# Kernel optimization log

Hardware: AMD Instinct MI355X
Metric: run time of the kernel (lower is better)

Reference implementation:

```python
import jax, jax.numpy as jnp
import numpy as np

DIM = 1024
NUM_HEADS = 16
HEAD_DIM = DIM // NUM_HEADS
SCALE = HEAD_DIM ** -0.5
B, LQ, LK = 2, 2048, 2048


def setup_inputs() -> dict:
    key = jax.random.key(0)
    ks = jax.random.split(key, 12)
    init = 1.0 / np.sqrt(DIM)  # ~ torch Linear default scale
    inp = {
        "q": jax.random.normal(ks[0], (B, LQ, DIM), jnp.float32),
        "k": jax.random.normal(ks[1], (B, LK, DIM), jnp.float32),
        "v": jax.random.normal(ks[2], (B, LK, DIM), jnp.float32),
        "kv_mask": jnp.ones((B, LK), jnp.int32),
        "Wq": jax.random.uniform(ks[3], (DIM, DIM), jnp.float32, -init, init),
        "bq": jax.random.uniform(ks[4], (DIM,), jnp.float32, -init, init),
        "Wk": jax.random.uniform(ks[5], (DIM, DIM), jnp.float32, -init, init),
        "bk": jax.random.uniform(ks[6], (DIM,), jnp.float32, -init, init),
        "Wv": jax.random.uniform(ks[7], (DIM, DIM), jnp.float32, -init, init),
        "bv": jax.random.uniform(ks[8], (DIM,), jnp.float32, -init, init),
        "Wo": jax.random.uniform(ks[9], (DIM, DIM), jnp.float32, -init, init),
        "bo": jax.random.uniform(ks[10], (DIM,), jnp.float32, -init, init),
    }
    return inp


def reference(q, k, v, kv_mask, Wq, bq, Wk, bk, Wv, bv, Wo, bo):
    Bq, Lq, D = q.shape
    Lk = k.shape[1]
    H, Hd = NUM_HEADS, HEAD_DIM
    # projections (torch Linear: x @ W.T + b); split heads -> [B, H, L, Hd]
    qh = (q @ Wq.T + bq).reshape(Bq, Lq, H, Hd).transpose(0, 2, 1, 3)
    kh = (k @ Wk.T + bk).reshape(Bq, Lk, H, Hd).transpose(0, 2, 1, 3)
    vh = (v @ Wv.T + bv).reshape(Bq, Lk, H, Hd).transpose(0, 2, 1, 3)
    # scores [B, H, Lq, Lk]
    attn = jnp.einsum("bhqd,bhkd->bhqk", qh, kh) * SCALE
    mask = (kv_mask != 0)[:, None, None, :]
    attn = jnp.where(mask, attn, -jnp.inf)
    attn = jax.nn.softmax(attn, axis=-1)
    # dropout is identity at inference (p applied only in train mode)
    out = jnp.einsum("bhqk,bhkd->bhqd", attn, vh)
    out = out.transpose(0, 2, 1, 3).reshape(Bq, Lq, D)
    return out @ Wo.T + bo
```

## Files before the change

kernel.cpp:

```cpp
#include <hip/hip_runtime.h>
#include <stdint.h>

typedef unsigned short u16;
typedef __attribute__((ext_vector_type(8))) __bf16 bf16x8;
typedef __attribute__((ext_vector_type(4))) float f32x4;

#define DIM 1024
#define NH 16
#define HD 64
#define BSZ 2
#define LQ 2048
#define LK 2048
#define SCALE_LOG2E 0.18033688011112043f
#define MNEG -3.0e38f


static __device__ __forceinline__ float b2f(u16 u) {
  union { uint32_t i; float f; } v; v.i = ((uint32_t)u) << 16; return v.f;
}
static __device__ __forceinline__ u16 f2b(float f) {
  uint32_t x = __float_as_uint(f);
  return (u16)((x + 0x7fffu + ((x >> 16) & 1u)) >> 16);
}
static __device__ __forceinline__ uint32_t pk2r(float lo, float hi) {
  uint32_t a = __float_as_uint(lo) + 0x8000u;
  uint32_t b = __float_as_uint(hi) + 0x8000u;
  return __builtin_amdgcn_perm(b, a, 0x07060302u);
}
static __device__ __forceinline__ f32x4 zero4() {
  f32x4 z; z[0] = 0.f; z[1] = 0.f; z[2] = 0.f; z[3] = 0.f; return z;
}
static __device__ __forceinline__ float exp2c(float s) {
  return exp2f(fminf(s, 30.0f));
}
static __device__ __forceinline__ void gload_lds16(const u16* g, u16* l) {
  __builtin_amdgcn_global_load_lds(
      (const __attribute__((address_space(1))) void*)g,
      (__attribute__((address_space(3))) void*)l, 16, 0, 0);
}

__global__ void mask_allvalid(const int* __restrict__ kvmask, int* allv) {
  int b = blockIdx.x;
  int base = b * LK + threadIdx.x * 8;
  int ok = 1;
#pragma unroll
  for (int j = 0; j < 8; ++j) ok &= (kvmask[base + j] != 0);
  unsigned long long m = __ballot(ok != 0);
  if ((threadIdx.x & 63) == 0 && m != ~0ULL) atomicAnd(&allv[b], 0);
}

struct ConvArgs {
  const float* src[11];
  long long cum[12];
  u16* dst;
};

__global__ void convert_inputs(ConvArgs ca) {
  long long c = (long long)blockIdx.x * blockDim.x + threadIdx.x;
  long long e0 = c * 8;
  if (e0 >= ca.cum[11]) return;
  int s = 0;
  while (e0 >= ca.cum[s + 1]) ++s;
  const float* sp = ca.src[s] + (e0 - ca.cum[s]);
  union { uint4 v; uint32_t w[4]; } t;
#pragma unroll
  for (int j = 0; j < 4; ++j) t.w[j] = pk2r(sp[2 * j], sp[2 * j + 1]);
  *(uint4*)(ca.dst + e0) = t.v;
}

struct GemmArgs {
  const u16* X[3];
  const u16* W[3];
  const u16* Bias[3];
  void* Y[3];
  float osc[3];
  int f32out;
  int vtz;
};

__global__ __launch_bounds__(256, 2) void gemm_bt_bias(GemmArgs ga) {
  const int K = DIM, N = DIM;
  __shared__ u16 smem[17408];
  u16* const Al = smem;
  u16* const Bl = smem + 8192;
  const int tid = threadIdx.x;
  const int wave = tid >> 6, lane = tid & 63;
  const int wm = wave >> 1, wn = wave & 1;
  const int lrow = lane & 15, quad = lane >> 4;
  const int z = blockIdx.z;
  const u16* X = ga.X[z];
  const u16* W = ga.W[z];
  const u16* Bias = ga.Bias[z];
  const float osc = ga.osc[z];
  const int m0 = blockIdx.x * 128;
  const int n0 = blockIdx.y * 128;

  f32x4 acc[4][4];
#pragma unroll
  for (int i = 0; i < 4; ++i)
#pragma unroll
    for (int j = 0; j < 4; ++j) acc[i][j] = zero4();

  const int cbase = wave * 256;
  for (int k0 = 0; k0 < K; k0 += 64) {
    __syncthreads();
#pragma unroll
    for (int i = 0; i < 4; ++i) {
      int c = cbase + i * 64 + lane;
      int row = c >> 3, colb = c & 7;
      gload_lds16(X + (size_t)(m0 + row) * K + k0 + colb * 8,
                  &Al[(cbase + i * 64) * 8]);
      gload_lds16(W + (size_t)(n0 + row) * K + k0 + colb * 8,
                  &Bl[(cbase + i * 64) * 8]);
    }
    __syncthreads();
#pragma unroll
    for (int ks = 0; ks < 2; ++ks) {
      bf16x8 af[4], bfr[4];
#pragma unroll
      for (int t = 0; t < 4; ++t)
        af[t] = *(const bf16x8*)&Al[(wm * 64 + t * 16 + lrow) * 64 + ks * 32 + quad * 8];
#pragma unroll
      for (int t = 0; t < 4; ++t)
        bfr[t] = *(const bf16x8*)&Bl[(wn * 64 + t * 16 + lrow) * 64 + ks * 32 + quad * 8];
#pragma unroll
      for (int mt = 0; mt < 4; ++mt)
#pragma unroll
        for (int nt = 0; nt < 4; ++nt)
          acc[mt][nt] = __builtin_amdgcn_mfma_f32_16x16x32_bf16(af[mt], bfr[nt], acc[mt][nt], 0, 0, 0);
    }
  }

  if (z == ga.vtz) {
    u16* Yv = (u16*)ga.Y[z];
    u16* const VT = smem;
    __syncthreads();
#pragma unroll
    for (int nt = 0; nt < 4; ++nt) {
      int colL = wn * 64 + nt * 16 + lrow;
      float bv = b2f(Bias[n0 + colL]);
#pragma unroll
      for (int mt = 0; mt < 4; ++mt) {
        int keyL = wm * 64 + mt * 16 + quad * 4;
        uint2 w;
        w.x = pk2r((acc[mt][nt][0] + bv) * osc, (acc[mt][nt][1] + bv) * osc);
        w.y = pk2r((acc[mt][nt][2] + bv) * osc, (acc[mt][nt][3] + bv) * osc);
        *(uint2*)&VT[colL * 136 + keyL] = w;
      }
    }
    __syncthreads();
    const int bb = m0 >> 11, key0 = m0 & 2047;
#pragma unroll
    for (int i = 0; i < 8; ++i) {
      int c = i * 256 + tid;
      int colL = c >> 4, k8 = c & 15;
      int hh = (n0 + colL) >> 6, dd = (n0 + colL) & 63;
      *(uint4*)(Yv + ((size_t)(bb * NH + hh) * HD + dd) * LK + key0 + k8 * 8) =
          *(const uint4*)&VT[colL * 136 + k8 * 8];
    }
  } else if (ga.f32out) {
    float* Yf = (float*)ga.Y[z];
#pragma unroll
    for (int nt = 0; nt < 4; ++nt) {
      int col = n0 + wn * 64 + nt * 16 + lrow;
      float bv = b2f(Bias[col]);
#pragma unroll
      for (int mt = 0; mt < 4; ++mt) {
        int rowb = m0 + wm * 64 + mt * 16 + quad * 4;
#pragma unroll
        for (int r = 0; r < 4; ++r)
          Yf[(size_t)(rowb + r) * N + col] = (acc[mt][nt][r] + bv) * osc;
      }
    }
  } else {
    u16* Yv = (u16*)ga.Y[z];
#pragma unroll
    for (int nt = 0; nt < 4; ++nt) {
      int col = n0 + wn * 64 + nt * 16 + lrow;
      float bv = b2f(Bias[col]);
#pragma unroll
      for (int mt = 0; mt < 4; ++mt) {
        int rowb = m0 + wm * 64 + mt * 16 + quad * 4;
#pragma unroll
        for (int r = 0; r < 4; ++r)
          Yv[(size_t)(rowb + r) * N + col] = f2b((acc[mt][nt][r] + bv) * osc);
      }
    }
  }
}

__global__ __launch_bounds__(256, 2) void attn_fused(
    const u16* __restrict__ qp, const u16* __restrict__ kp,
    const u16* __restrict__ vpt, const int* __restrict__ kvmask,
    const int* __restrict__ allv, u16* __restrict__ op) {
  __shared__ u16 Kl[128 * 72];
  __shared__ u16 Vt[64 * 136];
  __shared__ u16 Pp[4][32 * 40];
  __shared__ float Ml[128];
  const int tid = threadIdx.x;
  const int wave = tid >> 6, lane = tid & 63;
  const int lrow = lane & 15, quad = lane >> 4;
  const int bh = blockIdx.y;
  const int b = bh >> 4, h = bh & 15;
  const int q0 = blockIdx.x * 128;
  const bool av = (allv[b] != 0);

  const u16* qbase = qp + (size_t)b * LQ * DIM + h * HD;
  const u16* kbase = kp + (size_t)b * LK * DIM + h * HD;
  const u16* vtb = vpt + (size_t)(b * NH + h) * HD * LK;
  const int* mbase = kvmask + b * LK;
  const int wq0 = q0 + wave * 32;

  bf16x8 qf[2][2];
#pragma unroll
  for (int mt = 0; mt < 2; ++mt)
#pragma unroll
    for (int ks = 0; ks < 2; ++ks)
      qf[mt][ks] = *(const bf16x8*)(qbase + (size_t)(wq0 + mt * 16 + lrow) * DIM + ks * 32 + quad * 8);

  f32x4 acco[2][4];
  float lsum[2];
#pragma unroll
  for (int mt = 0; mt < 2; ++mt) {
#pragma unroll
    for (int dt = 0; dt < 4; ++dt) acco[mt][dt] = zero4();
    lsum[mt] = 0.0f;
  }

  const int kr_row = tid >> 3, kr_cb = (tid & 7) * 8;
  const int vr_d = tid >> 4, vr_k8 = (tid & 15) * 8;
  const u16* kptr = kbase + (size_t)kr_row * DIM + kr_cb;
  const u16* vptr = vtb + (size_t)vr_d * LK + vr_k8;
  u16* klds = &Kl[kr_row * 72 + kr_cb];
  u16* vlds = &Vt[vr_d * 136 + vr_k8];

  uint4 kr0, kr1, kr2, kr3, vr0, vr1, vr2, vr3;

  kr0 = *(const uint4*)(kptr);
  kr1 = *(const uint4*)(kptr + (size_t)32 * DIM);
  kr2 = *(const uint4*)(kptr + (size_t)64 * DIM);
  kr3 = *(const uint4*)(kptr + (size_t)96 * DIM);
  vr0 = *(const uint4*)(vptr);
  vr1 = *(const uint4*)(vptr + (size_t)16 * LK);
  vr2 = *(const uint4*)(vptr + (size_t)32 * LK);
  vr3 = *(const uint4*)(vptr + (size_t)48 * LK);
  *(uint4*)(klds) = kr0;
  *(uint4*)(klds + 32 * 72) = kr1;
  *(uint4*)(klds + 64 * 72) = kr2;
  *(uint4*)(klds + 96 * 72) = kr3;
  *(uint4*)(vlds) = vr0;
  *(uint4*)(vlds + 16 * 136) = vr1;
  *(uint4*)(vlds + 32 * 136) = vr2;
  *(uint4*)(vlds + 48 * 136) = vr3;
  if (!av && tid < 128) Ml[tid] = mbase[tid] ? 0.0f : MNEG;

  for (int kc = 0; kc < LK; kc += 128) {
    __syncthreads();
    const bool more = (kc + 128) < LK;

    if (more) {
      const u16* kp2 = kptr + (size_t)(kc + 128) * DIM;
      const u16* vp2 = vptr + (kc + 128);
      kr0 = *(const uint4*)(kp2);
      kr1 = *(const uint4*)(kp2 + (size_t)32 * DIM);
      kr2 = *(const uint4*)(kp2 + (size_t)64 * DIM);
      kr3 = *(const uint4*)(kp2 + (size_t)96 * DIM);
      vr0 = *(const uint4*)(vp2);
      vr1 = *(const uint4*)(vp2 + (size_t)16 * LK);
      vr2 = *(const uint4*)(vp2 + (size_t)32 * LK);
      vr3 = *(const uint4*)(vp2 + (size_t)48 * LK);
    }

    u16* pqw = &Pp[wave][0];
#pragma unroll
    for (int kb = 0; kb < 4; ++kb) {
      f32x4 sacc[2][2];
#pragma unroll
      for (int mt = 0; mt < 2; ++mt)
#pragma unroll
        for (int ntl = 0; ntl < 2; ++ntl) sacc[mt][ntl] = zero4();
#pragma unroll
      for (int ks = 0; ks < 2; ++ks) {
#pragma unroll
        for (int ntl = 0; ntl < 2; ++ntl) {
          bf16x8 kf = *(const bf16x8*)&Kl[((2 * kb + ntl) * 16 + lrow) * 72 + ks * 32 + quad * 8];
          sacc[0][ntl] = __builtin_amdgcn_mfma_f32_16x16x32_bf16(kf, qf[0][ks], sacc[0][ntl], 0, 0, 0);
          sacc[1][ntl] = __builtin_amdgcn_mfma_f32_16x16x32_bf16(kf, qf[1][ks], sacc[1][ntl], 0, 0, 0);
        }
      }

#pragma unroll
      for (int mt = 0; mt < 2; ++mt) {
        float rsum = 0.0f;
        u16* prow = &pqw[(mt * 16 + lrow) * 40];
        if (av) {
#pragma unroll
          for (int ntl = 0; ntl < 2; ++ntl) {
            float p0 = exp2c(sacc[mt][ntl][0]);
            float p1 = exp2c(sacc[mt][ntl][1]);
            float p2 = exp2c(sacc[mt][ntl][2]);
            float p3 = exp2c(sacc[mt][ntl][3]);
            rsum += (p0 + p1) + (p2 + p3);
            uint2 w; w.x = pk2r(p0, p1); w.y = pk2r(p2, p3);
            *(uint2*)&prow[ntl * 16 + quad * 4] = w;
          }
        } else {
#pragma unroll
          for (int ntl = 0; ntl < 2; ++ntl) {
            f32x4 mq = *(const f32x4*)&Ml[(2 * kb + ntl) * 16 + quad * 4];
            float p0 = exp2c(sacc[mt][ntl][0] + mq[0]);
            float p1 = exp2c(sacc[mt][ntl][1] + mq[1]);
            float p2 = exp2c(sacc[mt][ntl][2] + mq[2]);
            float p3 = exp2c(sacc[mt][ntl][3] + mq[3]);
            rsum += (p0 + p1) + (p2 + p3);
            uint2 w; w.x = pk2r(p0, p1); w.y = pk2r(p2, p3);
            *(uint2*)&prow[ntl * 16 + quad * 4] = w;
          }
        }
        lsum[mt] += rsum;
      }

      bf16x8 pf0 = *(const bf16x8*)&pqw[(0 * 16 + lrow) * 40 + quad * 8];
      bf16x8 pf1 = *(const bf16x8*)&pqw[(1 * 16 + lrow) * 40 + quad * 8];
#pragma unroll
      for (int dt = 0; dt < 4; ++dt) {
        bf16x8 vf = *(const bf16x8*)&Vt[(dt * 16 + lrow) * 136 + kb * 32 + quad * 8];
        acco[0][dt] = __builtin_amdgcn_mfma_f32_16x16x32_bf16(vf, pf0, acco[0][dt], 0, 0, 0);
        acco[1][dt] = __builtin_amdgcn_mfma_f32_16x16x32_bf16(vf, pf1, acco[1][dt], 0, 0, 0);
      }
    }

    __syncthreads();
    if (more) {
      *(uint4*)(klds) = kr0;
      *(uint4*)(klds + 32 * 72) = kr1;
      *(uint4*)(klds + 64 * 72) = kr2;
      *(uint4*)(klds + 96 * 72) = kr3;
      *(uint4*)(vlds) = vr0;
      *(uint4*)(vlds + 16 * 136) = vr1;
      *(uint4*)(vlds + 32 * 136) = vr2;
      *(uint4*)(vlds + 48 * 136) = vr3;
      if (!av && tid < 128) Ml[tid] = mbase[kc + 128 + tid] ? 0.0f : MNEG;
    }
  }

  u16* ob = op + (size_t)b * LQ * DIM + h * HD;
#pragma unroll
  for (int mt = 0; mt < 2; ++mt) {
    float t = lsum[mt];
    t += __shfl_xor(t, 16);
    t += __shfl_xor(t, 32);
    float inv = t > 0.0f ? 1.0f / t : 0.0f;
    int q = wq0 + mt * 16 + lrow;
#pragma unroll
    for (int dt = 0; dt < 4; ++dt) {
      uint2 w;
      w.x = pk2r(acco[mt][dt][0] * inv, acco[mt][dt][1] * inv);
      w.y = pk2r(acco[mt][dt][2] * inv, acco[mt][dt][3] * inv);
      *(uint2*)&ob[(size_t)q * DIM + dt * 16 + quad * 4] = w;
    }
  }
}

extern "C" void kernel_launch(void* const* d_in, const int* in_sizes, int n_in,
                              void* d_out, int out_size, void* d_ws, size_t ws_size,
                              hipStream_t stream) {
  (void)in_sizes; (void)n_in; (void)out_size; (void)ws_size;
  const int* kvmask = (const int*)d_in[3];

  u16* ws = (u16*)d_ws;
  const long long SQ = (long long)BSZ * LQ * DIM;
  const long long SW = (long long)DIM * DIM;
  const long long SB = DIM;
  long long cum[12];
  cum[0] = 0;
  cum[1] = cum[0] + SQ;
  cum[2] = cum[1] + SQ;
  cum[3] = cum[2] + SQ;
  cum[4] = cum[3] + SW;
  cum[5] = cum[4] + SW;
  cum[6] = cum[5] + SW;
  cum[7] = cum[6] + SW;
  cum[8] = cum[7] + SB;
  cum[9] = cum[8] + SB;
  cum[10] = cum[9] + SB;
  cum[11] = cum[10] + SB;
  const long long canon_end = cum[11];
  u16* cq  = ws + cum[0];
  u16* ck  = ws + cum[1];
  u16* cv  = ws + cum[2];
  u16* cWq = ws + cum[3];
  u16* cWk = ws + cum[4];
  u16* cWv = ws + cum[5];
  u16* cWo = ws + cum[6];
  u16* cbq = ws + cum[7];
  u16* cbk = ws + cum[8];
  u16* cbv = ws + cum[9];
  u16* cbo = ws + cum[10];
  u16* qp  = ws + canon_end;
  u16* kp  = qp + SQ;
  u16* vpt = kp + SQ;
  u16* ao  = vpt + SQ;
  int* allv = (int*)(ao + SQ);

  hipMemsetAsync(allv, 0xFF, 2 * sizeof(int), stream);
  mask_allvalid<<<BSZ, 256, 0, stream>>>(kvmask, allv);

  ConvArgs ca;
  ca.src[0] = (const float*)d_in[0];
  ca.src[1] = (const float*)d_in[1];
  ca.src[2] = (const float*)d_in[2];
  ca.src[3] = (const float*)d_in[4];
  ca.src[4] = (const float*)d_in[6];
  ca.src[5] = (const float*)d_in[8];
  ca.src[6] = (const float*)d_in[10];
  ca.src[7] = (const float*)d_in[5];
  ca.src[8] = (const float*)d_in[7];
  ca.src[9] = (const float*)d_in[9];
  ca.src[10] = (const float*)d_in[11];
  for (int i = 0; i < 12; ++i) ca.cum[i] = cum[i];
  ca.dst = ws;
  int conv_blocks = (int)((canon_end / 8 + 255) / 256);
  convert_inputs<<<conv_blocks, 256, 0, stream>>>(ca);

  const int M = BSZ * LQ;

  GemmArgs g1;
  g1.X[0] = cq; g1.W[0] = cWq; g1.Bias[0] = cbq; g1.Y[0] = qp;
  g1.X[1] = ck; g1.W[1] = cWk; g1.Bias[1] = cbk; g1.Y[1] = kp;
  g1.X[2] = cv; g1.W[2] = cWv; g1.Bias[2] = cbv; g1.Y[2] = vpt;
  g1.osc[0] = SCALE_LOG2E;
  g1.osc[1] = 1.0f;
  g1.osc[2] = 1.0f;
  g1.f32out = 0;
  g1.vtz = 2;
  gemm_bt_bias<<<dim3(M / 128, DIM / 128, 3), dim3(256), 0, stream>>>(g1);

  attn_fused<<<dim3(LQ / 128, BSZ * NH), dim3(256), 0, stream>>>(qp, kp, vpt, kvmask, allv, ao);

  GemmArgs g2;
  g2.X[0] = ao; g2.W[0] = cWo; g2.Bias[0] = cbo; g2.Y[0] = d_out;
  g2.X[1] = ao; g2.W[1] = cWo; g2.Bias[1] = cbo; g2.Y[1] = d_out;
  g2.X[2] = ao; g2.W[2] = cWo; g2.Bias[2] = cbo; g2.Y[2] = d_out;
  g2.osc[0] = 1.0f; g2.osc[1] = 1.0f; g2.osc[2] = 1.0f;
  g2.f32out = 1;
  g2.vtz = -1;
  gemm_bt_bias<<<dim3(M / 128, DIM / 128, 1), dim3(256), 0, stream>>>(g2);
}
```

Before: 266.3 us.

## Split attention over key range and merge partial sums; use raw v_exp_f32

The attention kernel gains a grid z-dimension that splits the key sequence in two. Each half writes unnormalized fp32 partial outputs and row sums to workspace, and a new merge kernel adds them and normalizes into bf16. The merge is a plain add with no max rescaling, which works because the kernel uses a fixed clamped exponent rather than a running max. The exp2 helper is also swapped for inline v_exp_f32 asm. The intent is more blocks for better CU utilization, paid for with extra fp32 partial traffic, an extra launch and duplicated Q loads; the split only runs when the workspace is large enough.

Measured after the change: 260.2 us. 1.02x faster.

```diff
diff --git a/kernel.cpp b/kernel.cpp
--- a/kernel.cpp
+++ b/kernel.cpp
@@ -31,12 +31,9 @@
   f32x4 z; z[0] = 0.f; z[1] = 0.f; z[2] = 0.f; z[3] = 0.f; return z;
 }
 static __device__ __forceinline__ float exp2c(float s) {
-  return exp2f(fminf(s, 30.0f));
-}
-static __device__ __forceinline__ void gload_lds16(const u16* g, u16* l) {
-  __builtin_amdgcn_global_load_lds(
-      (const __attribute__((address_space(1))) void*)g,
-      (__attribute__((address_space(3))) void*)l, 16, 0, 0);
+  float r;
+  asm("v_exp_f32 %0, %1\n\ts_nop 0" : "=v"(r) : "v"(fminf(s, 30.0f)));
+  return r;
 }
 
 __global__ void mask_allvalid(const int* __restrict__ kvmask, int* allv) {
@@ -77,6 +74,12 @@
   int f32out;
   int vtz;
 };
+
+static __device__ __forceinline__ void gload_lds16(const u16* g, u16* l) {
+  __builtin_amdgcn_global_load_lds(
+      (const __attribute__((address_space(1))) void*)g,
+      (__attribute__((address_space(3))) void*)l, 16, 0, 0);
+}
 
 __global__ __launch_bounds__(256, 2) void gemm_bt_bias(GemmArgs ga) {
   const int K = DIM, N = DIM;
@@ -192,7 +195,9 @@
 __global__ __launch_bounds__(256, 2) void attn_fused(
     const u16* __restrict__ qp, const u16* __restrict__ kp,
     const u16* __restrict__ vpt, const int* __restrict__ kvmask,
-    const int* __restrict__ allv, u16* __restrict__ op) {
+    const int* __restrict__ allv, u16* __restrict__ op,
+    float* __restrict__ opart, float* __restrict__ lpart,
+    int nsplit, int kspan) {
   __shared__ u16 Kl[128 * 72];
   __shared__ u16 Vt[64 * 136];
   __shared__ u16 Pp[4][32 * 40];
@@ -203,6 +208,8 @@
   const int bh = blockIdx.y;
   const int b = bh >> 4, h = bh & 15;
   const int q0 = blockIdx.x * 128;
+  const int kc0 = blockIdx.z * kspan;
+  const int kcend = kc0 + kspan;
   const bool av = (allv[b] != 0);
 
   const u16* qbase = qp + (size_t)b * LQ * DIM + h * HD;
@@ -236,14 +243,18 @@
 
   uint4 kr0, kr1, kr2, kr3, vr0, vr1, vr2, vr3;
 
-  kr0 = *(const uint4*)(kptr);
-  kr1 = *(const uint4*)(kptr + (size_t)32 * DIM);
-  kr2 = *(const uint4*)(kptr + (size_t)64 * DIM);
-  kr3 = *(const uint4*)(kptr + (size_t)96 * DIM);
-  vr0 = *(const uint4*)(vptr);
-  vr1 = *(const uint4*)(vptr + (size_t)16 * LK);
-  vr2 = *(const uint4*)(vptr + (size_t)32 * LK);
-  vr3 = *(const uint4*)(vptr + (size_t)48 * LK);
+  {
+    const u16* kp2 = kptr + (size_t)kc0 * DIM;
+    const u16* vp2 = vptr + kc0;
+    kr0 = *(const uint4*)(kp2);
+    kr1 = *(const uint4*)(kp2 + (size_t)32 * DIM);
+    kr2 = *(const uint4*)(kp2 + (size_t)64 * DIM);
+    kr3 = *(const uint4*)(kp2 + (size_t)96 * DIM);
+    vr0 = *(const uint4*)(vp2);
+    vr1 = *(const uint4*)(vp2 + (size_t)16 * LK);
+    vr2 = *(const uint4*)(vp2 + (size_t)32 * LK);
+    vr3 = *(const uint4*)(vp2 + (size_t)48 * LK);
+  }
   *(uint4*)(klds) = kr0;
   *(uint4*)(klds + 32 * 72) = kr1;
   *(uint4*)(klds + 64 * 72) = kr2;
@@ -252,11 +263,11 @@
   *(uint4*)(vlds + 16 * 136) = vr1;
   *(uint4*)(vlds + 32 * 136) = vr2;
   *(uint4*)(vlds + 48 * 136) = vr3;
-  if (!av && tid < 128) Ml[tid] = mbase[tid] ? 0.0f : MNEG;
-
-  for (int kc = 0; kc < LK; kc += 128) {
+  if (!av && tid < 128) Ml[tid] = mbase[kc0 + tid] ? 0.0f : MNEG;
+
+  for (int kc = kc0; kc < kcend; kc += 128) {
     __syncthreads();
-    const bool more = (kc + 128) < LK;
+    const bool more = (kc + 128) < kcend;
 
     if (more) {
       const u16* kp2 = kptr + (size_t)(kc + 128) * DIM;
@@ -344,28 +355,66 @@
     }
   }
 
-  u16* ob = op + (size_t)b * LQ * DIM + h * HD;
-#pragma unroll
-  for (int mt = 0; mt < 2; ++mt) {
-    float t = lsum[mt];
-    t += __shfl_xor(t, 16);
-    t += __shfl_xor(t, 32);
-    float inv = t > 0.0f ? 1.0f / t : 0.0f;
-    int q = wq0 + mt * 16 + lrow;
-#pragma unroll
-    for (int dt = 0; dt < 4; ++dt) {
-      uint2 w;
-      w.x = pk2r(acco[mt][dt][0] * inv, acco[mt][dt][1] * inv);
-      w.y = pk2r(acco[mt][dt][2] * inv, acco[mt][dt][3] * inv);
-      *(uint2*)&ob[(size_t)q * DIM + dt * 16 + quad * 4] = w;
-    }
-  }
+  if (nsplit == 2) {
+    const int sidx = blockIdx.z;
+    float* obs = opart + ((size_t)(sidx * BSZ + b) * LQ) * DIM + h * HD;
+    float* lps = lpart + ((size_t)(sidx * BSZ + b) * NH + h) * LQ;
+#pragma unroll
+    for (int mt = 0; mt < 2; ++mt) {
+      float t = lsum[mt];
+      t += __shfl_xor(t, 16);
+      t += __shfl_xor(t, 32);
+      int q = wq0 + mt * 16 + lrow;
+      if (quad == 0) lps[q] = t;
+#pragma unroll
+      for (int dt = 0; dt < 4; ++dt)
+        *(f32x4*)&obs[(size_t)q * DIM + dt * 16 + quad * 4] = acco[mt][dt];
+    }
+  } else {
+    u16* ob = op + (size_t)b * LQ * DIM + h * HD;
+#pragma unroll
+    for (int mt = 0; mt < 2; ++mt) {
+      float t = lsum[mt];
+      t += __shfl_xor(t, 16);
+      t += __shfl_xor(t, 32);
+      float inv = t > 0.0f ? 1.0f / t : 0.0f;
+      int q = wq0 + mt * 16 + lrow;
+#pragma unroll
+      for (int dt = 0; dt < 4; ++dt) {
+        uint2 w;
+        w.x = pk2r(acco[mt][dt][0] * inv, acco[mt][dt][1] * inv);
+        w.y = pk2r(acco[mt][dt][2] * inv, acco[mt][dt][3] * inv);
+        *(uint2*)&ob[(size_t)q * DIM + dt * 16 + quad * 4] = w;
+      }
+    }
+  }
+}
+
+__global__ void merge_splits(const float* __restrict__ opart,
+                             const float* __restrict__ lpart,
+                             u16* __restrict__ ao) {
+  size_t e = ((size_t)blockIdx.x * blockDim.x + threadIdx.x) * 4;
+  const size_t TOT = (size_t)BSZ * LQ * DIM;
+  if (e >= TOT) return;
+  int col = (int)(e % DIM);
+  int q = (int)((e / DIM) % LQ);
+  int b = (int)(e / ((size_t)LQ * DIM));
+  int h = col >> 6;
+  size_t li = ((size_t)b * NH + h) * LQ + q;
+  float l = lpart[li] + lpart[(size_t)BSZ * NH * LQ + li];
+  float inv = l > 0.0f ? 1.0f / l : 0.0f;
+  f32x4 a = *(const f32x4*)(opart + e);
+  f32x4 c = *(const f32x4*)(opart + TOT + e);
+  uint2 w;
+  w.x = pk2r((a[0] + c[0]) * inv, (a[1] + c[1]) * inv);
+  w.y = pk2r((a[2] + c[2]) * inv, (a[3] + c[3]) * inv);
+  *(uint2*)(ao + e) = w;
 }
 
 extern "C" void kernel_launch(void* const* d_in, const int* in_sizes, int n_in,
                               void* d_out, int out_size, void* d_ws, size_t ws_size,
                               hipStream_t stream) {
-  (void)in_sizes; (void)n_in; (void)out_size; (void)ws_size;
+  (void)in_sizes; (void)n_in; (void)out_size;
   const int* kvmask = (const int*)d_in[3];
 
   u16* ws = (u16*)d_ws;
@@ -403,6 +452,14 @@
   u16* ao  = vpt + SQ;
   int* allv = (int*)(ao + SQ);
 
+  uintptr_t fbase = (((uintptr_t)(allv + 4)) + 15) & ~(uintptr_t)15;
+  float* opart = (float*)fbase;
+  const size_t ON = (size_t)2 * BSZ * LQ * DIM;
+  const size_t LN = (size_t)2 * BSZ * NH * LQ;
+  float* lpart = opart + ON;
+  size_t need = (fbase - (uintptr_t)d_ws) + (ON + LN) * sizeof(float);
+  const int nsplit = (ws_size >= need) ? 2 : 1;
+
   hipMemsetAsync(allv, 0xFF, 2 * sizeof(int), stream);
   mask_allvalid<<<BSZ, 256, 0, stream>>>(kvmask, allv);
 
@@ -436,7 +493,12 @@
   g1.vtz = 2;
   gemm_bt_bias<<<dim3(M / 128, DIM / 128, 3), dim3(256), 0, stream>>>(g1);
 
-  attn_fused<<<dim3(LQ / 128, BSZ * NH), dim3(256), 0, stream>>>(qp, kp, vpt, kvmask, allv, ao);
+  attn_fused<<<dim3(LQ / 128, BSZ * NH, nsplit), dim3(256), 0, stream>>>(
+      qp, kp, vpt, kvmask, allv, ao, opart, lpart, nsplit, LK / nsplit);
+  if (nsplit == 2) {
+    int mblocks = (int)(((size_t)BSZ * LQ * DIM / 4 + 255) / 256);
+    merge_splits<<<mblocks, 256, 0, stream>>>(opart, lpart, ao);
+  }
 
   GemmArgs g2;
   g2.X[0] = ao; g2.W[0] = cWo; g2.Bias[0] = cbo; g2.Y[0] = d_out;
```
